# Kernel tuning notes

Measured on AMD Instinct MI355X. Metric: run time of the kernel, lower is better.

The kernel has to match this reference:

```python
import jax, jax.numpy as jnp
import numpy as np

SPARSITY = 5      # sparsity_level
DIAG_EPS = 1e-6   # max(epsilon, 1e-6) regularizer on gram_active
NORM_EPS = 1e-10  # epsilon used for atom normalization


def setup_inputs() -> dict:
    key = jax.random.key(0)
    kx, kd = jax.random.split(key)
    M, N, B = 64, 512, 65536
    X = jax.random.normal(kx, (M, B), dtype=jnp.float32)
    D = jax.random.normal(kd, (M, N), dtype=jnp.float32)
    # normalize_atoms=True: unit-L2 columns
    D = D / (jnp.linalg.norm(D, axis=0, keepdims=True) + NORM_EPS)
    return {"X": X, "D": D}


def reference(X, D):
    """Batched Orthogonal Matching Pursuit (KSVDDictionaryLearning.batch_omp).

    X: (M, B) signals, D: (M, N) column-normalized dictionary.
    Returns sparse coefficients (N, B) with SPARSITY nonzeros per column.
    """
    M, B = X.shape
    N = D.shape[1]
    gram = D.T @ D            # (N, N)
    dt_x_t = (D.T @ X).T      # (B, N)
    coeff = jnp.zeros((N, B), X.dtype)
    mask = jnp.zeros((N, B), dtype=bool)
    batch_idx = jnp.arange(B)
    selected = []
    for k in range(SPARSITY):  # fixed small unroll; active-set size grows k+1
        residual = X - D @ coeff                  # (M, B)
        corr = D.T @ residual                     # (N, B)
        corr = jnp.where(mask, 0.0, corr)
        idx = jnp.argmax(jnp.abs(corr), axis=0)   # (B,)
        selected.append(idx)
        mask = mask.at[idx, batch_idx].set(True)
        active = jnp.stack(selected, axis=1)      # (B, k+1)
        # gram restricted to active atoms: (B, k+1, k+1)
        gram_active = gram[active[:, :, None], active[:, None, :]]
        gram_active = gram_active + DIAG_EPS * jnp.eye(k + 1, dtype=gram.dtype)
        rhs = jnp.take_along_axis(dt_x_t, active, axis=1)          # (B, k+1)
        sol = jnp.linalg.solve(gram_active, rhs[..., None])[..., 0]  # (B, k+1)
        # rebuild coefficients: active covers every atom selected so far,
        # so scattering solutions into zeros matches the torch in-place writes
        coeff = jnp.zeros((N, B), X.dtype).at[active.T, batch_idx[None, :]].set(sol.T)
    return coeff
```

## Files before the change

kernel.cpp:

```cpp
#include <hip/hip_runtime.h>
#include <math.h>

#define NATOMS  512
#define MROWS   64
#define BATCH   65536
#define BT      4
#define NSPARSE 5
#define DEPS    1e-6

__global__ void ksvd_prep(const float* __restrict__ D,
                          float* __restrict__ gram) {
  const int idx = blockIdx.x * 256 + threadIdx.x;
  const int i = idx >> 9;
  const int j = idx & (NATOMS - 1);
  double acc = 0.0;
#pragma unroll 8
  for (int m = 0; m < MROWS; ++m)
    acc += (double)D[m * NATOMS + i] * (double)D[m * NATOMS + j];
  gram[idx] = (float)acc;
}

__global__ __launch_bounds__(256, 4) void ksvd_main(
    const float* __restrict__ X, const float* __restrict__ D,
    const float* __restrict__ gram, float* __restrict__ out) {
  __shared__ __align__(16) float xs[MROWS][BT];
  __shared__ __align__(16) float dtxT[BT][NATOMS + 8];

  const int t    = threadIdx.x;
  const int lane = t & 63;
  const int wave = t >> 6;
  const int b0   = blockIdx.x * BT;

  {
    const int m = t >> 2, c = t & 3;
    xs[m][c] = X[(size_t)m * BATCH + b0 + c];
  }
  __syncthreads();

  const int a0 = wave * 128 + 2 * lane;
  float accA[2][BT], accB[2][BT];
#pragma unroll
  for (int q = 0; q < 2; ++q)
#pragma unroll
    for (int c = 0; c < BT; ++c) { accA[q][c] = 0.0f; accB[q][c] = 0.0f; }

#pragma unroll 4
  for (int m = 0; m < MROWS; m += 2) {
    const float2 d0 = *reinterpret_cast<const float2*>(&D[m * NATOMS + a0]);
    const float2 d1 = *reinterpret_cast<const float2*>(&D[(m + 1) * NATOMS + a0]);
    const float4 xa = *reinterpret_cast<const float4*>(&xs[m][0]);
    const float4 xb = *reinterpret_cast<const float4*>(&xs[m + 1][0]);
    accA[0][0] += d0.x * xa.x; accA[0][1] += d0.x * xa.y;
    accA[0][2] += d0.x * xa.z; accA[0][3] += d0.x * xa.w;
    accA[1][0] += d0.y * xa.x; accA[1][1] += d0.y * xa.y;
    accA[1][2] += d0.y * xa.z; accA[1][3] += d0.y * xa.w;
    accB[0][0] += d1.x * xb.x; accB[0][1] += d1.x * xb.y;
    accB[0][2] += d1.x * xb.z; accB[0][3] += d1.x * xb.w;
    accB[1][0] += d1.y * xb.x; accB[1][1] += d1.y * xb.y;
    accB[1][2] += d1.y * xb.z; accB[1][3] += d1.y * xb.w;
  }
#pragma unroll
  for (int c = 0; c < BT; ++c) {
    dtxT[c][a0]     = accA[0][c] + accB[0][c];
    dtxT[c][a0 + 1] = accA[1][c] + accB[1][c];
  }
  __syncthreads();

  const int cglob = b0 + wave;
  double dtxd[8];
  {
    const float4 f0 = *reinterpret_cast<const float4*>(&dtxT[wave][8 * lane]);
    const float4 f1 = *reinterpret_cast<const float4*>(&dtxT[wave][8 * lane + 4]);
    dtxd[0] = (double)f0.x; dtxd[1] = (double)f0.y;
    dtxd[2] = (double)f0.z; dtxd[3] = (double)f0.w;
    dtxd[4] = (double)f1.x; dtxd[5] = (double)f1.y;
    dtxd[6] = (double)f1.z; dtxd[7] = (double)f1.w;
  }

  int    idxs[NSPARSE];
  float  rhsf[NSPARSE];
  float  gc[NSPARSE - 1][8];
  double L[NSPARSE][NSPARSE];
  double inv_d[NSPARSE];
  double y[NSPARSE];
  double sol[NSPARSE];

#pragma unroll
  for (int k = 0; k < NSPARSE; ++k) {
    float bv = -1.0f;
    int   bn = 0;
#pragma unroll
    for (int jj = 0; jj < 8; ++jj) {
      double cv = dtxd[jj];
#pragma unroll
      for (int s = 0; s < k; ++s) cv -= sol[s] * (double)gc[s][jj];
      const float av = fabsf((float)cv);
      if (av > bv) { bv = av; bn = 8 * lane + jj; }
    }
    float wmax = bv;
#pragma unroll
    for (int off = 1; off < 64; off <<= 1)
      wmax = fmaxf(wmax, __shfl_xor(wmax, off));
    const unsigned long long own = __ballot(bv == wmax);
    const int owner = __ffsll(own) - 1;
    int idx = __shfl(bn, owner);
    idx = __builtin_amdgcn_readfirstlane(idx);
    idxs[k] = idx;

    if (k < NSPARSE - 1) {
      const float4 g0 = *reinterpret_cast<const float4*>(
          &gram[(size_t)idx * NATOMS + 8 * lane]);
      const float4 g1 = *reinterpret_cast<const float4*>(
          &gram[(size_t)idx * NATOMS + 8 * lane + 4]);
      gc[k][0] = g0.x; gc[k][1] = g0.y; gc[k][2] = g0.z; gc[k][3] = g0.w;
      gc[k][4] = g1.x; gc[k][5] = g1.y; gc[k][6] = g1.z; gc[k][7] = g1.w;
    }

    rhsf[k] = dtxT[wave][idx];

    float arowf[NSPARSE];
#pragma unroll
    for (int j = 0; j < k; ++j)
      arowf[j] = gram[(size_t)idx * NATOMS + idxs[j]];
    const float gdiag = gram[(size_t)idx * NATOMS + idx];

    double ss = (double)gdiag + DEPS;
#pragma unroll
    for (int j = 0; j < k; ++j) {
      double w = (double)arowf[j];
#pragma unroll
      for (int tt = 0; tt < j; ++tt) w -= L[k][tt] * L[j][tt];
      w *= inv_d[j];
      L[k][j] = w;
      ss -= w * w;
    }
    const double inv = rsqrt(ss);
    L[k][k]  = ss * inv;
    inv_d[k] = inv;

    {
      double s2 = (double)rhsf[k];
#pragma unroll
      for (int j = 0; j < k; ++j) s2 -= L[k][j] * y[j];
      y[k] = s2 * inv;
    }
#pragma unroll
    for (int i = k; i >= 0; --i) {
      double s2 = y[i];
#pragma unroll
      for (int j = i + 1; j <= k; ++j) s2 -= L[j][i] * sol[j];
      sol[i] = s2 * inv_d[i];
    }
  }

  if (lane == 0) {
#pragma unroll
    for (int s = 0; s < NSPARSE; ++s)
      out[(size_t)idxs[s] * BATCH + cglob] = (float)sol[s];
  }
}

extern "C" void kernel_launch(void* const* d_in, const int* in_sizes, int n_in,
                              void* d_out, int out_size, void* d_ws,
                              size_t ws_size, hipStream_t stream) {
  (void)in_sizes; (void)n_in; (void)out_size; (void)ws_size;
  const float* X = (const float*)d_in[0];
  const float* D = (const float*)d_in[1];
  float* out = (float*)d_out;
  float* gram = (float*)d_ws;

  ksvd_prep<<<(NATOMS * NATOMS) / 256, 256, 0, stream>>>(D, gram);
  hipMemsetAsync(out, 0, (size_t)NATOMS * BATCH * sizeof(float), stream);
  ksvd_main<<<BATCH / BT, 256, 0, stream>>>(X, D, gram, out);
}
```

Measured before the change: 186.0 us.

## Fuse output zeroing into main kernel and process eight columns per block

Drops the separate memset: each block zeroes its own 8-column slice of the output with float4 stores before writing the sparse coefficients. Batch tile per block goes from 4 to 8, so the D^T X stage reuses each loaded D pair across more columns using packed float2 FMAs. Each wave now runs OMP for two columns in sequence, and the five results are written in parallel by lanes 0-4 instead of one lane. Zero stores and nonzero stores come from the same thread block, but ordering across different threads relies on global memory visibility. Doubling the work per wave halves the block count and lengthens the serial per-wave OMP chain.

```diff
diff --git a/kernel.cpp b/kernel.cpp
--- a/kernel.cpp
+++ b/kernel.cpp
@@ -4,9 +4,11 @@
 #define NATOMS  512
 #define MROWS   64
 #define BATCH   65536
-#define BT      4
+#define BT      8
 #define NSPARSE 5
 #define DEPS    1e-6
+
+typedef float v2f __attribute__((ext_vector_type(2)));
 
 __global__ void ksvd_prep(const float* __restrict__ D,
                           float* __restrict__ gram) {
@@ -23,8 +25,8 @@
 __global__ __launch_bounds__(256, 4) void ksvd_main(
     const float* __restrict__ X, const float* __restrict__ D,
     const float* __restrict__ gram, float* __restrict__ out) {
-  __shared__ __align__(16) float xs[MROWS][BT];
-  __shared__ __align__(16) float dtxT[BT][NATOMS + 8];
+  __shared__ __align__(16) v2f   xs2[MROWS][BT];
+  __shared__ __align__(16) float dtxT[BT][NATOMS + 4];
 
   const int t    = threadIdx.x;
   const int lane = t & 63;
@@ -32,131 +34,147 @@
   const int b0   = blockIdx.x * BT;
 
   {
-    const int m = t >> 2, c = t & 3;
-    xs[m][c] = X[(size_t)m * BATCH + b0 + c];
+    const int r0 = t >> 1;
+    const int h  = (t & 1) * 4;
+    const float4 z = {0.f, 0.f, 0.f, 0.f};
+#pragma unroll
+    for (int rr = 0; rr < 4; ++rr)
+      *reinterpret_cast<float4*>(
+          &out[(size_t)(r0 + 128 * rr) * BATCH + b0 + h]) = z;
+  }
+
+#pragma unroll
+  for (int e = t; e < MROWS * BT; e += 256) {
+    const int m = e >> 3, c = e & 7;
+    const float xv = X[(size_t)m * BATCH + b0 + c];
+    v2f p; p.x = xv; p.y = xv;
+    xs2[m][c] = p;
   }
   __syncthreads();
 
   const int a0 = wave * 128 + 2 * lane;
-  float accA[2][BT], accB[2][BT];
+  v2f accA[BT], accB[BT];
 #pragma unroll
-  for (int q = 0; q < 2; ++q)
-#pragma unroll
-    for (int c = 0; c < BT; ++c) { accA[q][c] = 0.0f; accB[q][c] = 0.0f; }
+  for (int c = 0; c < BT; ++c) {
+    accA[c].x = 0.f; accA[c].y = 0.f;
+    accB[c].x = 0.f; accB[c].y = 0.f;
+  }
 
 #pragma unroll 4
   for (int m = 0; m < MROWS; m += 2) {
-    const float2 d0 = *reinterpret_cast<const float2*>(&D[m * NATOMS + a0]);
-    const float2 d1 = *reinterpret_cast<const float2*>(&D[(m + 1) * NATOMS + a0]);
-    const float4 xa = *reinterpret_cast<const float4*>(&xs[m][0]);
-    const float4 xb = *reinterpret_cast<const float4*>(&xs[m + 1][0]);
-    accA[0][0] += d0.x * xa.x; accA[0][1] += d0.x * xa.y;
-    accA[0][2] += d0.x * xa.z; accA[0][3] += d0.x * xa.w;
-    accA[1][0] += d0.y * xa.x; accA[1][1] += d0.y * xa.y;
-    accA[1][2] += d0.y * xa.z; accA[1][3] += d0.y * xa.w;
-    accB[0][0] += d1.x * xb.x; accB[0][1] += d1.x * xb.y;
-    accB[0][2] += d1.x * xb.z; accB[0][3] += d1.x * xb.w;
-    accB[1][0] += d1.y * xb.x; accB[1][1] += d1.y * xb.y;
-    accB[1][2] += d1.y * xb.z; accB[1][3] += d1.y * xb.w;
+    const v2f dA = *reinterpret_cast<const v2f*>(&D[m * NATOMS + a0]);
+    const v2f dB = *reinterpret_cast<const v2f*>(&D[(m + 1) * NATOMS + a0]);
+#pragma unroll
+    for (int c = 0; c < BT; ++c) {
+      accA[c] = __builtin_elementwise_fma(dA, xs2[m][c],     accA[c]);
+      accB[c] = __builtin_elementwise_fma(dB, xs2[m + 1][c], accB[c]);
+    }
   }
 #pragma unroll
   for (int c = 0; c < BT; ++c) {
-    dtxT[c][a0]     = accA[0][c] + accB[0][c];
-    dtxT[c][a0 + 1] = accA[1][c] + accB[1][c];
+    const v2f s = accA[c] + accB[c];
+    *reinterpret_cast<v2f*>(&dtxT[c][a0]) = s;
   }
   __syncthreads();
 
-  const int cglob = b0 + wave;
-  double dtxd[8];
-  {
-    const float4 f0 = *reinterpret_cast<const float4*>(&dtxT[wave][8 * lane]);
-    const float4 f1 = *reinterpret_cast<const float4*>(&dtxT[wave][8 * lane + 4]);
-    dtxd[0] = (double)f0.x; dtxd[1] = (double)f0.y;
-    dtxd[2] = (double)f0.z; dtxd[3] = (double)f0.w;
-    dtxd[4] = (double)f1.x; dtxd[5] = (double)f1.y;
-    dtxd[6] = (double)f1.z; dtxd[7] = (double)f1.w;
-  }
+  for (int cc = 0; cc < 2; ++cc) {
+    const int cl    = 2 * wave + cc;
+    const int cglob = b0 + cl;
 
-  int    idxs[NSPARSE];
-  float  rhsf[NSPARSE];
-  float  gc[NSPARSE - 1][8];
-  double L[NSPARSE][NSPARSE];
-  double inv_d[NSPARSE];
-  double y[NSPARSE];
-  double sol[NSPARSE];
+    double dtxd[8];
+    {
+      const float4 f0 = *reinterpret_cast<const float4*>(&dtxT[cl][8 * lane]);
+      const float4 f1 = *reinterpret_cast<const float4*>(&dtxT[cl][8 * lane + 4]);
+      dtxd[0] = (double)f0.x; dtxd[1] = (double)f0.y;
+      dtxd[2] = (double)f0.z; dtxd[3] = (double)f0.w;
+      dtxd[4] = (double)f1.x; dtxd[5] = (double)f1.y;
+      dtxd[6] = (double)f1.z; dtxd[7] = (double)f1.w;
+    }
+
+    int    idxs[NSPARSE];
+    float  rhsf[NSPARSE];
+    float  gc[NSPARSE - 1][8];
+    double L[NSPARSE][NSPARSE];
+    double inv_d[NSPARSE];
+    double y[NSPARSE];
+    double sol[NSPARSE];
 
 #pragma unroll
-  for (int k = 0; k < NSPARSE; ++k) {
-    float bv = -1.0f;
-    int   bn = 0;
+    for (int k = 0; k < NSPARSE; ++k) {
+      float bv = -1.0f;
+      int   bn = 0;
 #pragma unroll
-    for (int jj = 0; jj < 8; ++jj) {
-      double cv = dtxd[jj];
+      for (int jj = 0; jj < 8; ++jj) {
+        double cv = dtxd[jj];
 #pragma unroll
-      for (int s = 0; s < k; ++s) cv -= sol[s] * (double)gc[s][jj];
-      const float av = fabsf((float)cv);
-      if (av > bv) { bv = av; bn = 8 * lane + jj; }
-    }
-    float wmax = bv;
+        for (int s = 0; s < k; ++s) cv -= sol[s] * (double)gc[s][jj];
+        const float av = fabsf((float)cv);
+        if (av > bv) { bv = av; bn = 8 * lane + jj; }
+      }
+      float wmax = bv;
 #pragma unroll
-    for (int off = 1; off < 64; off <<= 1)
-      wmax = fmaxf(wmax, __shfl_xor(wmax, off));
-    const unsigned long long own = __ballot(bv == wmax);
-    const int owner = __ffsll(own) - 1;
-    int idx = __shfl(bn, owner);
-    idx = __builtin_amdgcn_readfirstlane(idx);
-    idxs[k] = idx;
+      for (int off = 1; off < 64; off <<= 1)
+        wmax = fmaxf(wmax, __shfl_xor(wmax, off));
+      const unsigned long long own = __ballot(bv == wmax);
+      const int owner = __ffsll(own) - 1;
+      int idx = __shfl(bn, owner);
+      idx = __builtin_amdgcn_readfirstlane(idx);
+      idxs[k] = idx;
 
-    if (k < NSPARSE - 1) {
-      const float4 g0 = *reinterpret_cast<const float4*>(
-          &gram[(size_t)idx * NATOMS + 8 * lane]);
-      const float4 g1 = *reinterpret_cast<const float4*>(
-          &gram[(size_t)idx * NATOMS + 8 * lane + 4]);
-      gc[k][0] = g0.x; gc[k][1] = g0.y; gc[k][2] = g0.z; gc[k][3] = g0.w;
-      gc[k][4] = g1.x; gc[k][5] = g1.y; gc[k][6] = g1.z; gc[k][7] = g1.w;
+      if (k < NSPARSE - 1) {
+        const float4 g0 = *reinterpret_cast<const float4*>(
+            &gram[(size_t)idx * NATOMS + 8 * lane]);
+        const float4 g1 = *reinterpret_cast<const float4*>(
+            &gram[(size_t)idx * NATOMS + 8 * lane + 4]);
+        gc[k][0] = g0.x; gc[k][1] = g0.y; gc[k][2] = g0.z; gc[k][3] = g0.w;
+        gc[k][4] = g1.x; gc[k][5] = g1.y; gc[k][6] = g1.z; gc[k][7] = g1.w;
+      }
+
+      rhsf[k] = dtxT[cl][idx];
+
+      float arowf[NSPARSE];
+#pragma unroll
+      for (int j = 0; j < k; ++j)
+        arowf[j] = gram[(size_t)idx * NATOMS + idxs[j]];
+      const float gdiag = gram[(size_t)idx * NATOMS + idx];
+
+      double ss = (double)gdiag + DEPS;
+#pragma unroll
+      for (int j = 0; j < k; ++j) {
+        double w = (double)arowf[j];
+#pragma unroll
+        for (int tt = 0; tt < j; ++tt) w -= L[k][tt] * L[j][tt];
+        w *= inv_d[j];
+        L[k][j] = w;
+        ss -= w * w;
+      }
+      const double inv = rsqrt(ss);
+      L[k][k]  = ss * inv;
+      inv_d[k] = inv;
+
+      {
+        double s2 = (double)rhsf[k];
+#pragma unroll
+        for (int j = 0; j < k; ++j) s2 -= L[k][j] * y[j];
+        y[k] = s2 * inv;
+      }
+#pragma unroll
+      for (int i = k; i >= 0; --i) {
+        double s2 = y[i];
+#pragma unroll
+        for (int j = i + 1; j <= k; ++j) s2 -= L[j][i] * sol[j];
+        sol[i] = s2 * inv_d[i];
+      }
     }
 
-    rhsf[k] = dtxT[wave][idx];
-
-    float arowf[NSPARSE];
+    if (lane < NSPARSE) {
+      int    mi = idxs[0];
+      double ms = sol[0];
 #pragma unroll
-    for (int j = 0; j < k; ++j)
-      arowf[j] = gram[(size_t)idx * NATOMS + idxs[j]];
-    const float gdiag = gram[(size_t)idx * NATOMS + idx];
-
-    double ss = (double)gdiag + DEPS;
-#pragma unroll
-    for (int j = 0; j < k; ++j) {
-      double w = (double)arowf[j];
-#pragma unroll
-      for (int tt = 0; tt < j; ++tt) w -= L[k][tt] * L[j][tt];
-      w *= inv_d[j];
-      L[k][j] = w;
-      ss -= w * w;
+      for (int s = 1; s < NSPARSE; ++s)
+        if (lane == s) { mi = idxs[s]; ms = sol[s]; }
+      out[(size_t)mi * BATCH + cglob] = (float)ms;
     }
-    const double inv = rsqrt(ss);
-    L[k][k]  = ss * inv;
-    inv_d[k] = inv;
-
-    {
-      double s2 = (double)rhsf[k];
-#pragma unroll
-      for (int j = 0; j < k; ++j) s2 -= L[k][j] * y[j];
-      y[k] = s2 * inv;
-    }
-#pragma unroll
-    for (int i = k; i >= 0; --i) {
-      double s2 = y[i];
-#pragma unroll
-      for (int j = i + 1; j <= k; ++j) s2 -= L[j][i] * sol[j];
-      sol[i] = s2 * inv_d[i];
-    }
-  }
-
-  if (lane == 0) {
-#pragma unroll
-    for (int s = 0; s < NSPARSE; ++s)
-      out[(size_t)idxs[s] * BATCH + cglob] = (float)sol[s];
   }
 }
 
@@ -170,6 +188,5 @@
   float* gram = (float*)d_ws;
 
   ksvd_prep<<<(NATOMS * NATOMS) / 256, 256, 0, stream>>>(D, gram);
-  hipMemsetAsync(out, 0, (size_t)NATOMS * BATCH * sizeof(float), stream);
   ksvd_main<<<BATCH / BT, 256, 0, stream>>>(X, D, gram, out);
 }
```

After: 280.9 us. +51.0%, slower.

## Switch OMP solve to fp32 and use packed FMA for D^T X

Applied to the files above, without the earlier changes.

Replaces the double-precision correlation update, Cholesky factorization and triangular solves with fp32 arithmetic, avoiding the slower fp64 pipeline and the extra conversions. It also stores X pre-duplicated in shared memory so the D^T X accumulation can use two-wide packed FMAs on vector types, and reduces the padding on the dtxT shared array. The precision drop could change argmax tie-breaking or coefficient accuracy compared with the reference.

```diff
diff --git a/kernel.cpp b/kernel.cpp
--- a/kernel.cpp
+++ b/kernel.cpp
@@ -6,7 +6,9 @@
 #define BATCH   65536
 #define BT      4
 #define NSPARSE 5
-#define DEPS    1e-6
+#define DEPSF   1e-6f
+
+typedef float v2f __attribute__((ext_vector_type(2)));
 
 __global__ void ksvd_prep(const float* __restrict__ D,
                           float* __restrict__ gram) {
@@ -23,67 +25,72 @@
 __global__ __launch_bounds__(256, 4) void ksvd_main(
     const float* __restrict__ X, const float* __restrict__ D,
     const float* __restrict__ gram, float* __restrict__ out) {
-  __shared__ __align__(16) float xs[MROWS][BT];
-  __shared__ __align__(16) float dtxT[BT][NATOMS + 8];
+  __shared__ __align__(16) float4 xs4[MROWS][BT / 2];
+  __shared__ __align__(16) float  dtxT[BT][NATOMS + 4];
 
   const int t    = threadIdx.x;
   const int lane = t & 63;
   const int wave = t >> 6;
   const int b0   = blockIdx.x * BT;
 
-  {
-    const int m = t >> 2, c = t & 3;
-    xs[m][c] = X[(size_t)m * BATCH + b0 + c];
+  if (t < MROWS * 2) {
+    const int m = t >> 1, p = t & 1;
+    const float x0 = X[(size_t)m * BATCH + b0 + 2 * p];
+    const float x1 = X[(size_t)m * BATCH + b0 + 2 * p + 1];
+    float4 v; v.x = x0; v.y = x0; v.z = x1; v.w = x1;
+    xs4[m][p] = v;
   }
   __syncthreads();
 
   const int a0 = wave * 128 + 2 * lane;
-  float accA[2][BT], accB[2][BT];
+  v2f accA[BT], accB[BT];
 #pragma unroll
-  for (int q = 0; q < 2; ++q)
-#pragma unroll
-    for (int c = 0; c < BT; ++c) { accA[q][c] = 0.0f; accB[q][c] = 0.0f; }
+  for (int c = 0; c < BT; ++c) {
+    accA[c].x = 0.f; accA[c].y = 0.f;
+    accB[c].x = 0.f; accB[c].y = 0.f;
+  }
 
 #pragma unroll 4
   for (int m = 0; m < MROWS; m += 2) {
-    const float2 d0 = *reinterpret_cast<const float2*>(&D[m * NATOMS + a0]);
-    const float2 d1 = *reinterpret_cast<const float2*>(&D[(m + 1) * NATOMS + a0]);
-    const float4 xa = *reinterpret_cast<const float4*>(&xs[m][0]);
-    const float4 xb = *reinterpret_cast<const float4*>(&xs[m + 1][0]);
-    accA[0][0] += d0.x * xa.x; accA[0][1] += d0.x * xa.y;
-    accA[0][2] += d0.x * xa.z; accA[0][3] += d0.x * xa.w;
-    accA[1][0] += d0.y * xa.x; accA[1][1] += d0.y * xa.y;
-    accA[1][2] += d0.y * xa.z; accA[1][3] += d0.y * xa.w;
-    accB[0][0] += d1.x * xb.x; accB[0][1] += d1.x * xb.y;
-    accB[0][2] += d1.x * xb.z; accB[0][3] += d1.x * xb.w;
-    accB[1][0] += d1.y * xb.x; accB[1][1] += d1.y * xb.y;
-    accB[1][2] += d1.y * xb.z; accB[1][3] += d1.y * xb.w;
+    const v2f dA = *reinterpret_cast<const v2f*>(&D[m * NATOMS + a0]);
+    const v2f dB = *reinterpret_cast<const v2f*>(&D[(m + 1) * NATOMS + a0]);
+    const float4 xa0 = xs4[m][0];
+    const float4 xa1 = xs4[m][1];
+    const float4 xb0 = xs4[m + 1][0];
+    const float4 xb1 = xs4[m + 1][1];
+    v2f xv;
+    xv.x = xa0.x; xv.y = xa0.y; accA[0] = __builtin_elementwise_fma(dA, xv, accA[0]);
+    xv.x = xa0.z; xv.y = xa0.w; accA[1] = __builtin_elementwise_fma(dA, xv, accA[1]);
+    xv.x = xa1.x; xv.y = xa1.y; accA[2] = __builtin_elementwise_fma(dA, xv, accA[2]);
+    xv.x = xa1.z; xv.y = xa1.w; accA[3] = __builtin_elementwise_fma(dA, xv, accA[3]);
+    xv.x = xb0.x; xv.y = xb0.y; accB[0] = __builtin_elementwise_fma(dB, xv, accB[0]);
+    xv.x = xb0.z; xv.y = xb0.w; accB[1] = __builtin_elementwise_fma(dB, xv, accB[1]);
+    xv.x = xb1.x; xv.y = xb1.y; accB[2] = __builtin_elementwise_fma(dB, xv, accB[2]);
+    xv.x = xb1.z; xv.y = xb1.w; accB[3] = __builtin_elementwise_fma(dB, xv, accB[3]);
   }
 #pragma unroll
   for (int c = 0; c < BT; ++c) {
-    dtxT[c][a0]     = accA[0][c] + accB[0][c];
-    dtxT[c][a0 + 1] = accA[1][c] + accB[1][c];
+    const v2f s = accA[c] + accB[c];
+    *reinterpret_cast<v2f*>(&dtxT[c][a0]) = s;
   }
   __syncthreads();
 
   const int cglob = b0 + wave;
-  double dtxd[8];
+  float dtxr[8];
   {
     const float4 f0 = *reinterpret_cast<const float4*>(&dtxT[wave][8 * lane]);
     const float4 f1 = *reinterpret_cast<const float4*>(&dtxT[wave][8 * lane + 4]);
-    dtxd[0] = (double)f0.x; dtxd[1] = (double)f0.y;
-    dtxd[2] = (double)f0.z; dtxd[3] = (double)f0.w;
-    dtxd[4] = (double)f1.x; dtxd[5] = (double)f1.y;
-    dtxd[6] = (double)f1.z; dtxd[7] = (double)f1.w;
+    dtxr[0] = f0.x; dtxr[1] = f0.y; dtxr[2] = f0.z; dtxr[3] = f0.w;
+    dtxr[4] = f1.x; dtxr[5] = f1.y; dtxr[6] = f1.z; dtxr[7] = f1.w;
   }
 
-  int    idxs[NSPARSE];
-  float  rhsf[NSPARSE];
-  float  gc[NSPARSE - 1][8];
-  double L[NSPARSE][NSPARSE];
-  double inv_d[NSPARSE];
-  double y[NSPARSE];
-  double sol[NSPARSE];
+  int   idxs[NSPARSE];
+  float rhsf[NSPARSE];
+  float gc[NSPARSE - 1][8];
+  float L[NSPARSE][NSPARSE];
+  float inv_d[NSPARSE];
+  float y[NSPARSE];
+  float sol[NSPARSE];
 
 #pragma unroll
   for (int k = 0; k < NSPARSE; ++k) {
@@ -91,10 +98,10 @@
     int   bn = 0;
 #pragma unroll
     for (int jj = 0; jj < 8; ++jj) {
-      double cv = dtxd[jj];
+      float cv = dtxr[jj];
 #pragma unroll
-      for (int s = 0; s < k; ++s) cv -= sol[s] * (double)gc[s][jj];
-      const float av = fabsf((float)cv);
+      for (int s = 0; s < k; ++s) cv -= sol[s] * gc[s][jj];
+      const float av = fabsf(cv);
       if (av > bv) { bv = av; bn = 8 * lane + jj; }
     }
     float wmax = bv;
@@ -124,29 +131,29 @@
       arowf[j] = gram[(size_t)idx * NATOMS + idxs[j]];
     const float gdiag = gram[(size_t)idx * NATOMS + idx];
 
-    double ss = (double)gdiag + DEPS;
+    float ss = gdiag + DEPSF;
 #pragma unroll
     for (int j = 0; j < k; ++j) {
-      double w = (double)arowf[j];
+      float w = arowf[j];
 #pragma unroll
       for (int tt = 0; tt < j; ++tt) w -= L[k][tt] * L[j][tt];
       w *= inv_d[j];
       L[k][j] = w;
       ss -= w * w;
     }
-    const double inv = rsqrt(ss);
+    const float inv = rsqrtf(ss);
     L[k][k]  = ss * inv;
     inv_d[k] = inv;
 
     {
-      double s2 = (double)rhsf[k];
+      float s2 = rhsf[k];
 #pragma unroll
       for (int j = 0; j < k; ++j) s2 -= L[k][j] * y[j];
       y[k] = s2 * inv;
     }
 #pragma unroll
     for (int i = k; i >= 0; --i) {
-      double s2 = y[i];
+      float s2 = y[i];
 #pragma unroll
       for (int j = i + 1; j <= k; ++j) s2 -= L[j][i] * sol[j];
       sol[i] = s2 * inv_d[i];
@@ -156,7 +163,7 @@
   if (lane == 0) {
 #pragma unroll
     for (int s = 0; s < NSPARSE; ++s)
-      out[(size_t)idxs[s] * BATCH + cglob] = (float)sol[s];
+      out[(size_t)idxs[s] * BATCH + cglob] = sol[s];
   }
 }
 
```

After: 184.8 us. No clear change (-0.6%).
